# Kernel optimization log

Measured on AMD Instinct MI355X. Metric: run time of the kernel, lower is better.

Reference implementation:

```python
import jax, jax.numpy as jnp
import numpy as np

DECAY = 0.9      # decay_rate l
LR = 0.5         # fast-weight learning_rate e
STEP = 3         # inner-loop iterations
EPS = 1e-3       # keras LayerNormalization default epsilon

B, D_IN, U = 128, 256, 512


def setup_inputs() -> dict:
    key = jax.random.key(0)
    ks = jax.random.split(key, 6)
    return {
        "inputs": jax.random.normal(ks[0], (B, D_IN), dtype=jnp.float32),
        "prev_state": jax.random.normal(ks[1], (B, U), dtype=jnp.float32),
        "A": jax.random.normal(ks[2], (B, U, U), dtype=jnp.float32) * 0.01,
        "C": jax.random.normal(ks[3], (D_IN, U), dtype=jnp.float32) * (1.0 / np.sqrt(D_IN)),
        # original: glorot-identity init scaled by 0.05; randomized here, same math
        "W_h": jax.random.normal(ks[4], (U, U), dtype=jnp.float32) * 0.05,
        "bias": jax.random.normal(ks[5], (U,), dtype=jnp.float32) * 0.01,
        "gamma": jnp.ones((U,), dtype=jnp.float32),
        "beta": jnp.zeros((U,), dtype=jnp.float32),
    }


def _layer_norm(x, gamma, beta):
    m = jnp.mean(x, axis=-1, keepdims=True)
    v = jnp.var(x, axis=-1, keepdims=True)
    return (x - m) * jax.lax.rsqrt(v + EPS) * gamma + beta


def reference(inputs, prev_state, A, C, W_h, bias, gamma, beta):
    # slow path: h = act(prev @ W_h + x @ C + b)   -> [B, U]
    pre = prev_state @ W_h + inputs @ C
    h = jnp.tanh(pre + bias)
    # fast-weight update: A' = l*A + e * outer(h, h)  -> [B, U, U]
    A_new = DECAY * A + LR * jnp.einsum("bi,bj->bij", h, h)
    # inner loop: h_s = LN(act(prelim + h_s @ A'))  with h_s: [B, 1, U]
    prelim = pre[:, None, :]          # no bias / no activation, matching source
    h_s = h[:, None, :]
    for _ in range(STEP):
        h_s = jnp.tanh(prelim + jnp.einsum("bku,buv->bkv", h_s, A_new))
        h_s = _layer_norm(h_s, gamma, beta)
    out = h_s[:, 0, :]                # [B, U]; also the new recurrent state
    return out, A_new
```

## Files before the change

kernel.cpp:

```cpp
#include <hip/hip_runtime.h>
#include <math.h>

#define UDIM 512
#define DIN  256
#define BATCH 128
#define EPSV 1e-3f

#define NRSEG 8
#define RPB   64
#define HALFR 32

typedef float f4 __attribute__((ext_vector_type(4)));

__global__ __launch_bounds__(256) void k_pre(
    const float* __restrict__ inputs, const float* __restrict__ prev,
    const float* __restrict__ C, const float* __restrict__ Wh,
    const float* __restrict__ bias, float* __restrict__ pre, float* __restrict__ h)
{
    const int b = blockIdx.x >> 1;
    const int v = ((blockIdx.x & 1) << 8) + threadIdx.x;

    __shared__ float sprev[UDIM];
    __shared__ float sinp[DIN];
    for (int i = threadIdx.x; i < UDIM; i += 256) sprev[i] = prev[b * UDIM + i];
    sinp[threadIdx.x] = inputs[b * DIN + threadIdx.x];
    __syncthreads();

    float acc = 0.f;
#pragma unroll 8
    for (int u = 0; u < UDIM; ++u) acc = fmaf(sprev[u], Wh[u * UDIM + v], acc);
#pragma unroll 8
    for (int i = 0; i < DIN; ++i)  acc = fmaf(sinp[i], C[i * UDIM + v], acc);

    pre[b * UDIM + v] = acc;
    h[b * UDIM + v]   = tanhf(acc + bias[v]);
}

__global__ __launch_bounds__(256) void k_mv0ro(
    const float* __restrict__ A, const float* __restrict__ h,
    float* __restrict__ ypart, float* __restrict__ dotout)
{
    const int bc   = blockIdx.x;
    const int b    = bc >> 3;
    const int rs   = bc & 7;
    const int t    = threadIdx.x;
    const int lane = t & 63;
    const int wave = t >> 6;
    const int vg   = t & 127;
    const int col  = vg << 2;
    const int half = t >> 7;

    __shared__ __align__(16) float sh[UDIM];
    __shared__ __align__(16) float spart[2][UDIM];
    __shared__ float sred[4];

    sh[t]       = h[(size_t)b * UDIM + t];
    sh[t + 256] = h[(size_t)b * UDIM + t + 256];
    __syncthreads();

    float dp = sh[t] * sh[t] + sh[t + 256] * sh[t + 256];
#pragma unroll
    for (int off = 32; off; off >>= 1) dp += __shfl_xor(dp, off, 64);
    if (lane == 0) sred[wave] = dp;

    const int row0 = rs * RPB + half * HALFR;
    const float* __restrict__ Ab = A + ((size_t)b * UDIM + row0) * UDIM + col;

    f4 acc = {0.f, 0.f, 0.f, 0.f};
#pragma unroll 8
    for (int k = 0; k < HALFR; ++k) {
        const f4 a4 = *(const f4*)(Ab + (size_t)k * UDIM);
        const float hu = sh[row0 + k];
        acc.x = fmaf(hu, a4.x, acc.x);
        acc.y = fmaf(hu, a4.y, acc.y);
        acc.z = fmaf(hu, a4.z, acc.z);
        acc.w = fmaf(hu, a4.w, acc.w);
    }
    *(f4*)(&spart[half][col]) = acc;
    __syncthreads();

    {
        const float y0 = spart[0][t]       + spart[1][t];
        const float y1 = spart[0][t + 256] + spart[1][t + 256];
        ypart[(size_t)bc * UDIM + t]       = y0;
        ypart[(size_t)bc * UDIM + t + 256] = y1;
    }
    if (rs == 0 && t == 0)
        dotout[b] = sred[0] + sred[1] + sred[2] + sred[3];
}

__global__ __launch_bounds__(256) void k_mv(
    const float* __restrict__ A, float* __restrict__ Anew,
    const float* __restrict__ pre, const float* __restrict__ h,
    const float* __restrict__ ypin, const float* __restrict__ dotin,
    const float* __restrict__ gamma, const float* __restrict__ beta,
    float* __restrict__ ypout, float* __restrict__ dotout, const int wh)
{
    const int bc   = blockIdx.x;
    const int b    = bc >> 3;
    const int rs   = bc & 7;
    const int t    = threadIdx.x;
    const int lane = t & 63;
    const int wave = t >> 6;
    const int vg   = t & 127;
    const int col  = vg << 2;
    const int half = t >> 7;

    __shared__ __align__(16) float sh[UDIM];
    __shared__ __align__(16) float sx[UDIM];
    __shared__ float shs[UDIM];
    __shared__ __align__(16) float spart[2][UDIM];
    __shared__ float sred[8];
    __shared__ float sred2[4];
    __shared__ float sbc[2];

    sh[t]       = h[(size_t)b * UDIM + t];
    sh[t + 256] = h[(size_t)b * UDIM + t + 256];

    {
        float y0 = 0.f, y1 = 0.f;
#pragma unroll
        for (int s = 0; s < NRSEG; ++s) {
            y0 += ypin[((size_t)b * NRSEG + s) * UDIM + t];
            y1 += ypin[((size_t)b * NRSEG + s) * UDIM + t + 256];
        }
        const float d = 0.5f * dotin[b];
        y0 = fmaf(0.9f, y0, d * sh[t]);
        y1 = fmaf(0.9f, y1, d * sh[t + 256]);
        const float hs0 = tanhf(pre[(size_t)b * UDIM + t] + y0);
        const float hs1 = tanhf(pre[(size_t)b * UDIM + t + 256] + y1);
        shs[t] = hs0; shs[t + 256] = hs1;
        float s1 = hs0 + hs1, s2 = hs0 * hs0 + hs1 * hs1;
#pragma unroll
        for (int off = 32; off; off >>= 1) {
            s1 += __shfl_xor(s1, off, 64);
            s2 += __shfl_xor(s2, off, 64);
        }
        if (lane == 0) { sred[wave] = s1; sred[4 + wave] = s2; }
    }
    __syncthreads();
    if (t == 0) {
        float m = sred[0] + sred[1] + sred[2] + sred[3];
        float q = sred[4] + sred[5] + sred[6] + sred[7];
        m *= (1.f / UDIM);
        q = q * (1.f / UDIM) - m * m;
        sbc[0] = m;
        sbc[1] = rsqrtf(q + EPSV);
    }
    __syncthreads();
    {
        const float m = sbc[0], r = sbc[1];
        sx[t]       = (shs[t]       - m) * r * gamma[t]       + beta[t];
        sx[t + 256] = (shs[t + 256] - m) * r * gamma[t + 256] + beta[t + 256];
    }
    __syncthreads();

    {
        float dp = sx[t] * sh[t] + sx[t + 256] * sh[t + 256];
#pragma unroll
        for (int off = 32; off; off >>= 1) dp += __shfl_xor(dp, off, 64);
        if (lane == 0) sred2[wave] = dp;
    }

    const int row0 = rs * RPB + half * HALFR;
    const float* __restrict__ Ab  = A    + ((size_t)b * UDIM + row0) * UDIM + col;
    float*       __restrict__ Anb = Anew + ((size_t)b * UDIM + row0) * UDIM + col;
    const f4 hv4 = *(const f4*)(sh + col);

    f4 acc = {0.f, 0.f, 0.f, 0.f};
    if (half == wh) {
#pragma unroll 8
        for (int k = 0; k < HALFR; ++k) {
            const f4 a4 = *(const f4*)(Ab + (size_t)k * UDIM);
            const float xu = sx[row0 + k];
            const float s  = 0.5f * sh[row0 + k];
            f4 an;
            an.x = fmaf(s, hv4.x, 0.9f * a4.x);
            an.y = fmaf(s, hv4.y, 0.9f * a4.y);
            an.z = fmaf(s, hv4.z, 0.9f * a4.z);
            an.w = fmaf(s, hv4.w, 0.9f * a4.w);
            __builtin_nontemporal_store(an, (f4*)(Anb + (size_t)k * UDIM));
            acc.x = fmaf(xu, a4.x, acc.x);
            acc.y = fmaf(xu, a4.y, acc.y);
            acc.z = fmaf(xu, a4.z, acc.z);
            acc.w = fmaf(xu, a4.w, acc.w);
        }
    } else {
#pragma unroll 8
        for (int k = 0; k < HALFR; ++k) {
            const f4 a4 = *(const f4*)(Ab + (size_t)k * UDIM);
            const float xu = sx[row0 + k];
            acc.x = fmaf(xu, a4.x, acc.x);
            acc.y = fmaf(xu, a4.y, acc.y);
            acc.z = fmaf(xu, a4.z, acc.z);
            acc.w = fmaf(xu, a4.w, acc.w);
        }
    }
    *(f4*)(&spart[half][col]) = acc;
    __syncthreads();

    {
        const float y0 = spart[0][t]       + spart[1][t];
        const float y1 = spart[0][t + 256] + spart[1][t + 256];
        ypout[(size_t)bc * UDIM + t]       = y0;
        ypout[(size_t)bc * UDIM + t + 256] = y1;
    }
    if (rs == 0 && t == 0)
        dotout[b] = sred2[0] + sred2[1] + sred2[2] + sred2[3];
}

__global__ __launch_bounds__(512) void k_fin(
    const float* __restrict__ pre, const float* __restrict__ h,
    const float* __restrict__ ypin, const float* __restrict__ dotin,
    const float* __restrict__ gamma, const float* __restrict__ beta,
    float* __restrict__ out)
{
    const int b    = blockIdx.x;
    const int t    = threadIdx.x;
    const int lane = t & 63;
    const int wave = t >> 6;

    __shared__ float sred[16];
    __shared__ float sbc[2];

    float y = 0.f;
#pragma unroll
    for (int s = 0; s < NRSEG; ++s) y += ypin[((size_t)b * NRSEG + s) * UDIM + t];
    y = fmaf(0.9f, y, 0.5f * dotin[b] * h[(size_t)b * UDIM + t]);
    const float hs = tanhf(pre[(size_t)b * UDIM + t] + y);

    float s1 = hs, s2 = hs * hs;
#pragma unroll
    for (int off = 32; off; off >>= 1) {
        s1 += __shfl_xor(s1, off, 64);
        s2 += __shfl_xor(s2, off, 64);
    }
    if (lane == 0) { sred[wave] = s1; sred[8 + wave] = s2; }
    __syncthreads();
    if (t == 0) {
        float m = 0.f, q = 0.f;
#pragma unroll
        for (int i = 0; i < 8; ++i) { m += sred[i]; q += sred[8 + i]; }
        m *= (1.f / UDIM);
        q = q * (1.f / UDIM) - m * m;
        sbc[0] = m;
        sbc[1] = rsqrtf(q + EPSV);
    }
    __syncthreads();
    out[(size_t)b * UDIM + t] = (hs - sbc[0]) * sbc[1] * gamma[t] + beta[t];
}

extern "C" void kernel_launch(void* const* d_in, const int* in_sizes, int n_in,
                              void* d_out, int out_size, void* d_ws, size_t ws_size,
                              hipStream_t stream) {
    const float* inputs = (const float*)d_in[0];
    const float* prev   = (const float*)d_in[1];
    const float* A      = (const float*)d_in[2];
    const float* C      = (const float*)d_in[3];
    const float* Wh     = (const float*)d_in[4];
    const float* bias   = (const float*)d_in[5];
    const float* gamma  = (const float*)d_in[6];
    const float* beta   = (const float*)d_in[7];

    float* out  = (float*)d_out;
    float* Anew = out + (size_t)BATCH * UDIM;

    float* pre  = (float*)d_ws;
    float* h    = pre  + (size_t)BATCH * UDIM;
    float* ypA  = h    + (size_t)BATCH * UDIM;
    float* ypB  = ypA  + (size_t)BATCH * NRSEG * UDIM;
    float* dotH = ypB  + (size_t)BATCH * NRSEG * UDIM;
    float* dot1 = dotH + BATCH;
    float* dot2 = dot1 + BATCH;

    k_pre  <<<BATCH * 2, 256, 0, stream>>>(inputs, prev, C, Wh, bias, pre, h);
    k_mv0ro<<<BATCH * NRSEG, 256, 0, stream>>>(A, h, ypA, dotH);
    k_mv   <<<BATCH * NRSEG, 256, 0, stream>>>(A, Anew, pre, h, ypA, dotH,
                                               gamma, beta, ypB, dot1, 0);
    k_mv   <<<BATCH * NRSEG, 256, 0, stream>>>(A, Anew, pre, h, ypB, dot1,
                                               gamma, beta, ypA, dot2, 1);
    k_fin  <<<BATCH, 512, 0, stream>>>(pre, h, ypA, dot2, gamma, beta, out);
}
```

Baseline: 131.1 us.

## Write A_new in first pass and reread a bf16 copy of A in later iterations

The first matvec kernel now also writes A_new and, when the workspace is large enough, a bf16 copy of A. The two later inner-loop matvec kernels read the half-size bf16 copy instead of re-streaming the fp32 A. Writing A_new moves out of the iteration kernels into the first pass. The goal is to cut HBM read traffic in the memory-bound iterations, at the cost of an extra bf16 write and reduced precision in the h_s @ A products. Accuracy may drift relative to the fp32 reference.

```diff
diff --git a/kernel.cpp b/kernel.cpp
--- a/kernel.cpp
+++ b/kernel.cpp
@@ -5,12 +5,19 @@
 #define DIN  256
 #define BATCH 128
 #define EPSV 1e-3f
-
-#define NRSEG 8
+#define NSLAB 8
 #define RPB   64
-#define HALFR 32
 
 typedef float f4 __attribute__((ext_vector_type(4)));
+typedef unsigned int  u32;
+typedef unsigned int  u4  __attribute__((ext_vector_type(4)));
+typedef unsigned short us4 __attribute__((ext_vector_type(4)));
+
+__device__ inline unsigned short f2bf(float f) {
+    u32 u = __float_as_uint(f);
+    u32 r = u + 0x7fffu + ((u >> 16) & 1u);
+    return (unsigned short)(r >> 16);
+}
 
 __global__ __launch_bounds__(256) void k_pre(
     const float* __restrict__ inputs, const float* __restrict__ prev,
@@ -36,8 +43,10 @@
     h[b * UDIM + v]   = tanhf(acc + bias[v]);
 }
 
-__global__ __launch_bounds__(256) void k_mv0ro(
+template <int WBF>
+__global__ __launch_bounds__(256) void k_p0(
     const float* __restrict__ A, const float* __restrict__ h,
+    float* __restrict__ Anew, us4* __restrict__ Abf,
     float* __restrict__ ypart, float* __restrict__ dotout)
 {
     const int bc   = blockIdx.x;
@@ -49,6 +58,7 @@
     const int vg   = t & 127;
     const int col  = vg << 2;
     const int half = t >> 7;
+    const int row0 = rs * RPB + half * 32;
 
     __shared__ __align__(16) float sh[UDIM];
     __shared__ __align__(16) float spart[2][UDIM];
@@ -63,14 +73,29 @@
     for (int off = 32; off; off >>= 1) dp += __shfl_xor(dp, off, 64);
     if (lane == 0) sred[wave] = dp;
 
-    const int row0 = rs * RPB + half * HALFR;
-    const float* __restrict__ Ab = A + ((size_t)b * UDIM + row0) * UDIM + col;
+    const f4 hv4 = *(const f4*)(sh + col);
+    const float* __restrict__ Ab  = A    + ((size_t)b * UDIM + row0) * UDIM + col;
+    float*       __restrict__ Anb = Anew + ((size_t)b * UDIM + row0) * UDIM + col;
+    us4*         __restrict__ Bfb = WBF ? (Abf + (((size_t)b * UDIM + row0) * UDIM + col) / 4) : nullptr;
 
     f4 acc = {0.f, 0.f, 0.f, 0.f};
-#pragma unroll 8
-    for (int k = 0; k < HALFR; ++k) {
-        const f4 a4 = *(const f4*)(Ab + (size_t)k * UDIM);
+#pragma unroll 4
+    for (int k = 0; k < 32; ++k) {
+        const f4 a4 = __builtin_nontemporal_load((const f4*)(Ab + (size_t)k * UDIM));
         const float hu = sh[row0 + k];
+        const float s  = 0.5f * hu;
+        f4 an;
+        an.x = fmaf(s, hv4.x, 0.9f * a4.x);
+        an.y = fmaf(s, hv4.y, 0.9f * a4.y);
+        an.z = fmaf(s, hv4.z, 0.9f * a4.z);
+        an.w = fmaf(s, hv4.w, 0.9f * a4.w);
+        __builtin_nontemporal_store(an, (f4*)(Anb + (size_t)k * UDIM));
+        if (WBF) {
+            us4 bv;
+            bv.x = f2bf(a4.x); bv.y = f2bf(a4.y);
+            bv.z = f2bf(a4.z); bv.w = f2bf(a4.w);
+            Bfb[(size_t)k * (UDIM / 4)] = bv;
+        }
         acc.x = fmaf(hu, a4.x, acc.x);
         acc.y = fmaf(hu, a4.y, acc.y);
         acc.z = fmaf(hu, a4.z, acc.z);
@@ -79,22 +104,119 @@
     *(f4*)(&spart[half][col]) = acc;
     __syncthreads();
 
-    {
-        const float y0 = spart[0][t]       + spart[1][t];
-        const float y1 = spart[0][t + 256] + spart[1][t + 256];
-        ypart[(size_t)bc * UDIM + t]       = y0;
-        ypart[(size_t)bc * UDIM + t + 256] = y1;
-    }
+    ypart[(size_t)bc * UDIM + t]       = spart[0][t]       + spart[1][t];
+    ypart[(size_t)bc * UDIM + t + 256] = spart[0][t + 256] + spart[1][t + 256];
     if (rs == 0 && t == 0)
         dotout[b] = sred[0] + sred[1] + sred[2] + sred[3];
 }
 
-__global__ __launch_bounds__(256) void k_mv(
-    const float* __restrict__ A, float* __restrict__ Anew,
+__device__ inline void combine_ln(
+    int b, int t, int lane, int wave,
     const float* __restrict__ pre, const float* __restrict__ h,
     const float* __restrict__ ypin, const float* __restrict__ dotin,
     const float* __restrict__ gamma, const float* __restrict__ beta,
-    float* __restrict__ ypout, float* __restrict__ dotout, const int wh)
+    float* sx, float* sred, float* sred2, float* sbc)
+{
+    float y0 = 0.f, y1 = 0.f;
+#pragma unroll
+    for (int s = 0; s < NSLAB; ++s) {
+        y0 += ypin[((size_t)b * NSLAB + s) * UDIM + t];
+        y1 += ypin[((size_t)b * NSLAB + s) * UDIM + t + 256];
+    }
+    const float h0 = h[(size_t)b * UDIM + t];
+    const float h1 = h[(size_t)b * UDIM + t + 256];
+    const float d  = 0.5f * dotin[b];
+    y0 = fmaf(0.9f, y0, d * h0);
+    y1 = fmaf(0.9f, y1, d * h1);
+    const float hs0 = tanhf(pre[(size_t)b * UDIM + t]       + y0);
+    const float hs1 = tanhf(pre[(size_t)b * UDIM + t + 256] + y1);
+    float s1 = hs0 + hs1, s2 = hs0 * hs0 + hs1 * hs1;
+#pragma unroll
+    for (int off = 32; off; off >>= 1) {
+        s1 += __shfl_xor(s1, off, 64);
+        s2 += __shfl_xor(s2, off, 64);
+    }
+    if (lane == 0) { sred[wave] = s1; sred[4 + wave] = s2; }
+    __syncthreads();
+    if (t == 0) {
+        float m = sred[0] + sred[1] + sred[2] + sred[3];
+        float q = sred[4] + sred[5] + sred[6] + sred[7];
+        m *= (1.f / UDIM);
+        q = q * (1.f / UDIM) - m * m;
+        sbc[0] = m;
+        sbc[1] = rsqrtf(q + EPSV);
+    }
+    __syncthreads();
+    const float m = sbc[0], r = sbc[1];
+    const float x0 = (hs0 - m) * r * gamma[t]       + beta[t];
+    const float x1 = (hs1 - m) * r * gamma[t + 256] + beta[t + 256];
+    sx[t] = x0; sx[t + 256] = x1;
+    float dp = x0 * h0 + x1 * h1;
+#pragma unroll
+    for (int off = 32; off; off >>= 1) dp += __shfl_xor(dp, off, 64);
+    if (lane == 0) sred2[wave] = dp;
+    __syncthreads();
+}
+
+__global__ __launch_bounds__(256) void k_mv_bf(
+    const u4* __restrict__ Abf, const float* __restrict__ pre,
+    const float* __restrict__ h, const float* __restrict__ ypin,
+    const float* __restrict__ dotin, const float* __restrict__ gamma,
+    const float* __restrict__ beta, float* __restrict__ ypout,
+    float* __restrict__ dotout)
+{
+    const int bc   = blockIdx.x;
+    const int b    = bc >> 3;
+    const int rs   = bc & 7;
+    const int t    = threadIdx.x;
+    const int lane = t & 63;
+    const int wave = t >> 6;
+
+    __shared__ __align__(16) float sx[UDIM];
+    __shared__ __align__(16) float spart[4][UDIM];
+    __shared__ float sred[8], sred2[4], sbc[2];
+
+    combine_ln(b, t, lane, wave, pre, h, ypin, dotin, gamma, beta,
+               sx, sred, sred2, sbc);
+    if (rs == 0 && t == 0)
+        dotout[b] = sred2[0] + sred2[1] + sred2[2] + sred2[3];
+
+    const int cg  = t & 63;
+    const int qtr = t >> 6;
+    const int row0 = rs * RPB + qtr * 16;
+    const u4* __restrict__ Ab = Abf + (size_t)(b * UDIM + row0) * (UDIM / 8) + cg;
+
+    float a0=0,a1=0,a2=0,a3=0,a4a=0,a5=0,a6=0,a7=0;
+#pragma unroll 4
+    for (int k = 0; k < 16; ++k) {
+        const u4 q = Ab[(size_t)k * (UDIM / 8)];
+        const float xu = sx[row0 + k];
+        a0 = fmaf(xu, __uint_as_float(q.x << 16),        a0);
+        a1 = fmaf(xu, __uint_as_float(q.x & 0xFFFF0000u), a1);
+        a2 = fmaf(xu, __uint_as_float(q.y << 16),        a2);
+        a3 = fmaf(xu, __uint_as_float(q.y & 0xFFFF0000u), a3);
+        a4a= fmaf(xu, __uint_as_float(q.z << 16),        a4a);
+        a5 = fmaf(xu, __uint_as_float(q.z & 0xFFFF0000u), a5);
+        a6 = fmaf(xu, __uint_as_float(q.w << 16),        a6);
+        a7 = fmaf(xu, __uint_as_float(q.w & 0xFFFF0000u), a7);
+    }
+    f4 lo = {a0, a1, a2, a3}, hi = {a4a, a5, a6, a7};
+    *(f4*)(&spart[qtr][cg * 8])     = lo;
+    *(f4*)(&spart[qtr][cg * 8 + 4]) = hi;
+    __syncthreads();
+
+    ypout[(size_t)bc * UDIM + t] =
+        spart[0][t] + spart[1][t] + spart[2][t] + spart[3][t];
+    ypout[(size_t)bc * UDIM + t + 256] =
+        spart[0][t+256] + spart[1][t+256] + spart[2][t+256] + spart[3][t+256];
+}
+
+__global__ __launch_bounds__(256) void k_mv_f32(
+    const float* __restrict__ A, const float* __restrict__ pre,
+    const float* __restrict__ h, const float* __restrict__ ypin,
+    const float* __restrict__ dotin, const float* __restrict__ gamma,
+    const float* __restrict__ beta, float* __restrict__ ypout,
+    float* __restrict__ dotout)
 {
     const int bc   = blockIdx.x;
     const int b    = bc >> 3;
@@ -105,108 +227,33 @@
     const int vg   = t & 127;
     const int col  = vg << 2;
     const int half = t >> 7;
-
-    __shared__ __align__(16) float sh[UDIM];
+    const int row0 = rs * RPB + half * 32;
+
     __shared__ __align__(16) float sx[UDIM];
-    __shared__ float shs[UDIM];
     __shared__ __align__(16) float spart[2][UDIM];
-    __shared__ float sred[8];
-    __shared__ float sred2[4];
-    __shared__ float sbc[2];
-
-    sh[t]       = h[(size_t)b * UDIM + t];
-    sh[t + 256] = h[(size_t)b * UDIM + t + 256];
-
-    {
-        float y0 = 0.f, y1 = 0.f;
-#pragma unroll
-        for (int s = 0; s < NRSEG; ++s) {
-            y0 += ypin[((size_t)b * NRSEG + s) * UDIM + t];
-            y1 += ypin[((size_t)b * NRSEG + s) * UDIM + t + 256];
-        }
-        const float d = 0.5f * dotin[b];
-        y0 = fmaf(0.9f, y0, d * sh[t]);
-        y1 = fmaf(0.9f, y1, d * sh[t + 256]);
-        const float hs0 = tanhf(pre[(size_t)b * UDIM + t] + y0);
-        const float hs1 = tanhf(pre[(size_t)b * UDIM + t + 256] + y1);
-        shs[t] = hs0; shs[t + 256] = hs1;
-        float s1 = hs0 + hs1, s2 = hs0 * hs0 + hs1 * hs1;
-#pragma unroll
-        for (int off = 32; off; off >>= 1) {
-            s1 += __shfl_xor(s1, off, 64);
-            s2 += __shfl_xor(s2, off, 64);
-        }
-        if (lane == 0) { sred[wave] = s1; sred[4 + wave] = s2; }
-    }
-    __syncthreads();
-    if (t == 0) {
-        float m = sred[0] + sred[1] + sred[2] + sred[3];
-        float q = sred[4] + sred[5] + sred[6] + sred[7];
-        m *= (1.f / UDIM);
-        q = q * (1.f / UDIM) - m * m;
-        sbc[0] = m;
-        sbc[1] = rsqrtf(q + EPSV);
-    }
-    __syncthreads();
-    {
-        const float m = sbc[0], r = sbc[1];
-        sx[t]       = (shs[t]       - m) * r * gamma[t]       + beta[t];
-        sx[t + 256] = (shs[t + 256] - m) * r * gamma[t + 256] + beta[t + 256];
-    }
-    __syncthreads();
-
-    {
-        float dp = sx[t] * sh[t] + sx[t + 256] * sh[t + 256];
-#pragma unroll
-        for (int off = 32; off; off >>= 1) dp += __shfl_xor(dp, off, 64);
-        if (lane == 0) sred2[wave] = dp;
-    }
-
-    const int row0 = rs * RPB + half * HALFR;
-    const float* __restrict__ Ab  = A    + ((size_t)b * UDIM + row0) * UDIM + col;
-    float*       __restrict__ Anb = Anew + ((size_t)b * UDIM + row0) * UDIM + col;
-    const f4 hv4 = *(const f4*)(sh + col);
-
-    f4 acc = {0.f, 0.f, 0.f, 0.f};
-    if (half == wh) {
-#pragma unroll 8
-        for (int k = 0; k < HALFR; ++k) {
-            const f4 a4 = *(const f4*)(Ab + (size_t)k * UDIM);
-            const float xu = sx[row0 + k];
-            const float s  = 0.5f * sh[row0 + k];
-            f4 an;
-            an.x = fmaf(s, hv4.x, 0.9f * a4.x);
-            an.y = fmaf(s, hv4.y, 0.9f * a4.y);
-            an.z = fmaf(s, hv4.z, 0.9f * a4.z);
-            an.w = fmaf(s, hv4.w, 0.9f * a4.w);
-            __builtin_nontemporal_store(an, (f4*)(Anb + (size_t)k * UDIM));
-            acc.x = fmaf(xu, a4.x, acc.x);
-            acc.y = fmaf(xu, a4.y, acc.y);
-            acc.z = fmaf(xu, a4.z, acc.z);
-            acc.w = fmaf(xu, a4.w, acc.w);
-        }
-    } else {
-#pragma unroll 8
-        for (int k = 0; k < HALFR; ++k) {
-            const f4 a4 = *(const f4*)(Ab + (size_t)k * UDIM);
-            const float xu = sx[row0 + k];
-            acc.x = fmaf(xu, a4.x, acc.x);
-            acc.y = fmaf(xu, a4.y, acc.y);
-            acc.z = fmaf(xu, a4.z, acc.z);
-            acc.w = fmaf(xu, a4.w, acc.w);
-        }
-    }
-    *(f4*)(&spart[half][col]) = acc;
-    __syncthreads();
-
-    {
-        const float y0 = spart[0][t]       + spart[1][t];
-        const float y1 = spart[0][t + 256] + spart[1][t + 256];
-        ypout[(size_t)bc * UDIM + t]       = y0;
-        ypout[(size_t)bc * UDIM + t + 256] = y1;
-    }
+    __shared__ float sred[8], sred2[4], sbc[2];
+
+    combine_ln(b, t, lane, wave, pre, h, ypin, dotin, gamma, beta,
+               sx, sred, sred2, sbc);
     if (rs == 0 && t == 0)
         dotout[b] = sred2[0] + sred2[1] + sred2[2] + sred2[3];
+
+    const float* __restrict__ Ab = A + ((size_t)b * UDIM + row0) * UDIM + col;
+    f4 acc = {0.f, 0.f, 0.f, 0.f};
+#pragma unroll 4
+    for (int k = 0; k < 32; ++k) {
+        const f4 a4 = *(const f4*)(Ab + (size_t)k * UDIM);
+        const float xu = sx[row0 + k];
+        acc.x = fmaf(xu, a4.x, acc.x);
+        acc.y = fmaf(xu, a4.y, acc.y);
+        acc.z = fmaf(xu, a4.z, acc.z);
+        acc.w = fmaf(xu, a4.w, acc.w);
+    }
+    *(f4*)(&spart[half][col]) = acc;
+    __syncthreads();
+
+    ypout[(size_t)bc * UDIM + t]       = spart[0][t]       + spart[1][t];
+    ypout[(size_t)bc * UDIM + t + 256] = spart[0][t + 256] + spart[1][t + 256];
 }
 
 __global__ __launch_bounds__(512) void k_fin(
@@ -225,7 +272,7 @@
 
     float y = 0.f;
 #pragma unroll
-    for (int s = 0; s < NRSEG; ++s) y += ypin[((size_t)b * NRSEG + s) * UDIM + t];
+    for (int s = 0; s < NSLAB; ++s) y += ypin[((size_t)b * NSLAB + s) * UDIM + t];
     y = fmaf(0.9f, y, 0.5f * dotin[b] * h[(size_t)b * UDIM + t]);
     const float hs = tanhf(pre[(size_t)b * UDIM + t] + y);
 
@@ -268,16 +315,30 @@
     float* pre  = (float*)d_ws;
     float* h    = pre  + (size_t)BATCH * UDIM;
     float* ypA  = h    + (size_t)BATCH * UDIM;
-    float* ypB  = ypA  + (size_t)BATCH * NRSEG * UDIM;
-    float* dotH = ypB  + (size_t)BATCH * NRSEG * UDIM;
+    float* ypB  = ypA  + (size_t)BATCH * NSLAB * UDIM;
+    float* dotH = ypB  + (size_t)BATCH * NSLAB * UDIM;
     float* dot1 = dotH + BATCH;
     float* dot2 = dot1 + BATCH;
-
-    k_pre  <<<BATCH * 2, 256, 0, stream>>>(inputs, prev, C, Wh, bias, pre, h);
-    k_mv0ro<<<BATCH * NRSEG, 256, 0, stream>>>(A, h, ypA, dotH);
-    k_mv   <<<BATCH * NRSEG, 256, 0, stream>>>(A, Anew, pre, h, ypA, dotH,
-                                               gamma, beta, ypB, dot1, 0);
-    k_mv   <<<BATCH * NRSEG, 256, 0, stream>>>(A, Anew, pre, h, ypB, dot1,
-                                               gamma, beta, ypA, dot2, 1);
-    k_fin  <<<BATCH, 512, 0, stream>>>(pre, h, ypA, dot2, gamma, beta, out);
-}
+    char*  abf  = (char*)(dot2 + BATCH);
+    size_t aoff = ((size_t)abf + 15) & ~(size_t)15;
+    us4*   Abf  = (us4*)aoff;
+    const size_t need = (aoff - (size_t)d_ws) + (size_t)BATCH * UDIM * UDIM * 2;
+    const bool useBf = (ws_size >= need);
+
+    k_pre<<<BATCH * 2, 256, 0, stream>>>(inputs, prev, C, Wh, bias, pre, h);
+
+    if (useBf) {
+        k_p0<1><<<BATCH * NSLAB, 256, 0, stream>>>(A, h, Anew, Abf, ypA, dotH);
+        k_mv_bf<<<BATCH * NSLAB, 256, 0, stream>>>((const u4*)Abf, pre, h, ypA,
+                                                   dotH, gamma, beta, ypB, dot1);
+        k_mv_bf<<<BATCH * NSLAB, 256, 0, stream>>>((const u4*)Abf, pre, h, ypB,
+                                                   dot1, gamma, beta, ypA, dot2);
+    } else {
+        k_p0<0><<<BATCH * NSLAB, 256, 0, stream>>>(A, h, Anew, nullptr, ypA, dotH);
+        k_mv_f32<<<BATCH * NSLAB, 256, 0, stream>>>(A, pre, h, ypA,
+                                                    dotH, gamma, beta, ypB, dot1);
+        k_mv_f32<<<BATCH * NSLAB, 256, 0, stream>>>(A, pre, h, ypB,
+                                                    dot1, gamma, beta, ypA, dot2);
+    }
+    k_fin<<<BATCH, 512, 0, stream>>>(pre, h, ypA, dot2, gamma, beta, out);
+}
```

Result: faster. 127.2 us (-3.0%).
